# Kernel optimization log

Hardware: AMD Instinct MI355X
Metric: run time of the kernel (lower is better)

## Reference

```python
import jax, jax.numpy as jnp
import numpy as np

D_MODEL = 1024
N_HEADS = 16
D_HEAD = D_MODEL // N_HEADS
NEG_INF = -1000000000.0


def setup_inputs() -> dict:
    key = jax.random.key(0)
    ks = jax.random.split(key, 12)
    B, S1, S2 = 2, 2048, 2048
    query = jax.random.normal(ks[0], (B, S1, D_MODEL), dtype=jnp.float32)
    k_in = jax.random.normal(ks[1], (B, S2, D_MODEL), dtype=jnp.float32)
    v_in = jax.random.normal(ks[2], (B, S2, D_MODEL), dtype=jnp.float32)
    # causal mask: True = position is masked out (filled with -1e9)
    mask = jnp.broadcast_to(jnp.triu(jnp.ones((S1, S2), dtype=bool), k=1), (B, S1, S2))
    s = 1.0 / np.sqrt(D_MODEL)
    W_q = jax.random.uniform(ks[3], (D_MODEL, D_MODEL), jnp.float32, -s, s)
    b_q = jax.random.uniform(ks[4], (D_MODEL,), jnp.float32, -s, s)
    W_k = jax.random.uniform(ks[5], (D_MODEL, D_MODEL), jnp.float32, -s, s)
    b_k = jax.random.uniform(ks[6], (D_MODEL,), jnp.float32, -s, s)
    W_v = jax.random.uniform(ks[7], (D_MODEL, D_MODEL), jnp.float32, -s, s)
    b_v = jax.random.uniform(ks[8], (D_MODEL,), jnp.float32, -s, s)
    W_o = jax.random.uniform(ks[9], (D_MODEL, D_MODEL), jnp.float32, -s, s)
    b_o = jax.random.uniform(ks[10], (D_MODEL,), jnp.float32, -s, s)
    return {"query": query, "key": k_in, "value": v_in, "mask": mask,
            "W_q": W_q, "b_q": b_q, "W_k": W_k, "b_k": b_k,
            "W_v": W_v, "b_v": b_v, "W_o": W_o, "b_o": b_o}


def reference(query, key, value, mask, W_q, b_q, W_k, b_k, W_v, b_v, W_o, b_o):
    B, S1, _ = query.shape
    S2 = key.shape[1]
    scalar = 1.0 / np.sqrt(D_HEAD)
    # projections (torch Linear: x @ W.T + b)
    Q = (query @ W_q.T + b_q).reshape(B, S1, N_HEADS, D_HEAD).transpose(0, 2, 1, 3)
    K = (key @ W_k.T + b_k).reshape(B, S2, N_HEADS, D_HEAD).transpose(0, 2, 1, 3)
    V = (value @ W_v.T + b_v).reshape(B, S2, N_HEADS, D_HEAD).transpose(0, 2, 1, 3)
    # [B, H, S1, S2]
    scores = jnp.einsum('bhqd,bhkd->bhqk', Q, K) * scalar
    scores = jnp.where(mask[:, None, :, :], NEG_INF, scores)
    probs = jax.nn.softmax(scores, axis=-1)
    attn = jnp.einsum('bhqk,bhkd->bhqd', probs, V)
    concat = attn.transpose(0, 2, 1, 3).reshape(B, S1, D_MODEL)
    return concat @ W_o.T + b_o
```

## Files before the change

### kernel.cpp

```cpp
#include <hip/hip_runtime.h>
#include <hip/hip_bf16.h>
#include <stdint.h>

typedef __bf16 bf16;
typedef __bf16 bf16x8 __attribute__((ext_vector_type(8)));
typedef float f32x4 __attribute__((ext_vector_type(4)));
typedef float f32x16 __attribute__((ext_vector_type(16)));
typedef unsigned int u32;
typedef u32 u32x4 __attribute__((ext_vector_type(4)));

#define D_MODEL 1024
#define S_LEN 2048
#define NB 2
#define NH 16
#define DH 64

__device__ __forceinline__ void gload_lds16(const bf16* g, bf16* l) {
    auto gp = reinterpret_cast<const __attribute__((address_space(1))) unsigned int*>(
        reinterpret_cast<uintptr_t>(g));
    auto lp = reinterpret_cast<__attribute__((address_space(3))) unsigned int*>(
        reinterpret_cast<uintptr_t>(l));
    __builtin_amdgcn_global_load_lds(gp, lp, 16, 0, 0);
}

__device__ __forceinline__ u32 cvtpk(float lo, float hi) {
    u32 r; asm("v_cvt_pk_bf16_f32 %0, %1, %2" : "=v"(r) : "v"(lo), "v"(hi)); return r;
}
__device__ __forceinline__ void plswap(u32& a, u32& b) {
    asm("v_permlane32_swap_b32 %0, %1" : "+v"(a), "+v"(b));
}

__global__ __launch_bounds__(256)
void cvt_all(const float* __restrict__ q, const float* __restrict__ k,
             const float* __restrict__ v, const float* __restrict__ w0,
             const float* __restrict__ w1, const float* __restrict__ w2,
             const float* __restrict__ w3,
             bf16* __restrict__ oq, bf16* __restrict__ ok, bf16* __restrict__ ov,
             bf16* __restrict__ o0, bf16* __restrict__ o1, bf16* __restrict__ o2,
             bf16* __restrict__ o3)
{
    const int bid = blockIdx.x;
    const float* in; bf16* out; int local;
    if (bid < 6144) {
        int r = bid >> 11; local = bid & 2047;
        in  = (r == 0) ? q  : (r == 1) ? k  : v;
        out = (r == 0) ? oq : (r == 1) ? ok : ov;
    } else {
        int wb = bid - 6144;
        int r = wb >> 9; local = wb & 511;
        in  = (r == 0) ? w0 : (r == 1) ? w1 : (r == 2) ? w2 : w3;
        out = (r == 0) ? o0 : (r == 1) ? o1 : (r == 2) ? o2 : o3;
    }
    const size_t i = ((size_t)local * 256 + threadIdx.x) * 8;
    f32x4 x = *(const f32x4*)(in + i);
    f32x4 y = *(const f32x4*)(in + i + 4);
    bf16x8 o;
    #pragma unroll
    for (int j = 0; j < 4; ++j) { o[j] = (bf16)x[j]; o[4 + j] = (bf16)y[j]; }
    *(bf16x8*)(out + i) = o;
}

template<int OUT_F32, int TRANS>
__global__ __launch_bounds__(256)
void gemm_bf16(const bf16* __restrict__ Ap, const bf16* __restrict__ Bp,
               const float* __restrict__ bias, void* __restrict__ Cp,
               int M, int N, int K, float cscale)
{
    __shared__ __align__(16) bf16 As[2][128 * 64];
    __shared__ __align__(16) bf16 Bs[2][64 * 64];

    const int t = threadIdx.x, lane = t & 63, wid = t >> 6;
    const int nbn = N >> 6;
    const int cpx = gridDim.x >> 3;
    const int bid = blockIdx.x;
    const int swz = (bid & 7) * cpx + (bid >> 3);
    const int bm0 = (swz / nbn) << 7;
    const int bn0 = (swz % nbn) << 6;
    const int r16 = lane & 15, g = lane >> 4;
    const int wr = (wid >> 1) << 6;
    const int wc = (wid & 1) << 5;

    f32x4 acc[4][2] = {};

    auto stage = [&](int buf, int k0) {
        #pragma unroll
        for (int i = 0; i < 4; ++i) {
            int ch = wid * 256 + i * 64 + lane;
            int row = ch >> 3, c8 = ch & 7;
            int sc = c8 ^ (row & 7);
            gload_lds16(Ap + (size_t)(bm0 + row) * K + k0 + sc * 8, &As[buf][ch * 8]);
        }
        #pragma unroll
        for (int i = 0; i < 2; ++i) {
            int ch = wid * 128 + i * 64 + lane;
            int row = ch >> 3, c8 = ch & 7;
            int sc = c8 ^ (row & 7);
            gload_lds16(Bp + (size_t)(bn0 + row) * K + k0 + sc * 8, &Bs[buf][ch * 8]);
        }
    };

    int cur = 0;
    stage(0, 0);
    for (int k0 = 0; k0 < K; k0 += 64) {
        __syncthreads();
        if (k0 + 64 < K) stage(cur ^ 1, k0 + 64);
        #pragma unroll
        for (int ks = 0; ks < 2; ++ks) {
            const int cl = ks * 4 + g;
            bf16x8 af[4], bfr[2];
            #pragma unroll
            for (int mi = 0; mi < 4; ++mi) {
                int row = wr + mi * 16 + r16;
                af[mi] = *(const bf16x8*)((const char*)&As[cur][0] + row * 128 + ((cl ^ (row & 7)) << 4));
            }
            #pragma unroll
            for (int ni = 0; ni < 2; ++ni) {
                int row = wc + ni * 16 + r16;
                bfr[ni] = *(const bf16x8*)((const char*)&Bs[cur][0] + row * 128 + ((cl ^ (row & 7)) << 4));
            }
            #pragma unroll
            for (int mi = 0; mi < 4; ++mi)
                #pragma unroll
                for (int ni = 0; ni < 2; ++ni)
                    acc[mi][ni] = __builtin_amdgcn_mfma_f32_16x16x32_bf16(af[mi], bfr[ni], acc[mi][ni], 0, 0, 0);
        }
        cur ^= 1;
    }

    const int rb = g * 4;
    if (TRANS) {
        __syncthreads();
        bf16* Ts = (bf16*)&As[0][0];
        #pragma unroll
        for (int mi = 0; mi < 4; ++mi)
            #pragma unroll
            for (int ni = 0; ni < 2; ++ni) {
                int dl = wc + ni * 16 + r16;
                float bv = bias[bn0 + dl];
                #pragma unroll
                for (int r = 0; r < 4; ++r) {
                    int sl = wr + mi * 16 + rb + r;
                    Ts[dl * 136 + sl] = (bf16)(acc[mi][ni][r] + bv);
                }
            }
        __syncthreads();
        const int bq = bm0 >> 11, hq = bn0 >> 6, s0 = bm0 & 2047;
        bf16* VT = (bf16*)Cp;
        #pragma unroll
        for (int i2 = 0; i2 < 4; ++i2) {
            int ch = t + i2 * 256;
            int d = ch >> 4, sc = ch & 15;
            bf16x8 v = *(const bf16x8*)&Ts[d * 136 + sc * 8];
            *(bf16x8*)(VT + ((size_t)(bq * 16 + hq) * 64 + d) * S_LEN + s0 + sc * 8) = v;
        }
    } else {
        #pragma unroll
        for (int mi = 0; mi < 4; ++mi) {
            #pragma unroll
            for (int ni = 0; ni < 2; ++ni) {
                int cg = bn0 + wc + ni * 16 + r16;
                float bv = bias[cg];
                #pragma unroll
                for (int r = 0; r < 4; ++r) {
                    int rg = bm0 + wr + mi * 16 + rb + r;
                    float v = (acc[mi][ni][r] + bv) * cscale;
                    if (OUT_F32) ((float*)Cp)[(size_t)rg * N + cg] = v;
                    else         ((bf16*)Cp)[(size_t)rg * N + cg] = (bf16)v;
                }
            }
        }
    }
}

__global__ __launch_bounds__(256, 2)
void attn5(const bf16* __restrict__ Qp, const bf16* __restrict__ Kp,
           const bf16* __restrict__ VTp, bf16* __restrict__ Op)
{
    __shared__ __align__(16) char smem[32768];

    const int t = threadIdx.x, lane = t & 63, qs = t >> 6;
    const int l31 = lane & 31, hh = lane >> 5;

    const int bid = blockIdx.x;
    const int xcd = bid & 7, slot = bid >> 3;
    const int bh = xcd * 4 + (slot & 3);
    const int sh = slot >> 2;
    const int qt = (sh < 8) ? (15 - sh) : (sh - 8);
    const int b = bh >> 4, h = bh & 15;

    const size_t base = (size_t)b * (S_LEN * D_MODEL) + h * DH;
    const size_t vtbase = (size_t)bh * (DH * S_LEN);

    const int q0b = qt * 128;
    const int q0w = q0b + qs * 32;
    const int NT = 2 * qt + 2;
    const int teff = 2 * qt + (qs >> 1) + 1;

    const int ch0 = t, ch1 = t + 256;
    const int row0 = ch0 >> 3, ssc0 = ((ch0 & 7) ^ (row0 & 7)) << 3;
    const int row1 = ch1 >> 3, ssc1 = ((ch1 & 7) ^ (row1 & 7)) << 3;

    auto stage = [&](int buf, int tt) {
        char* kb = smem + buf * 16384;
        char* vb = kb + 8192;
        gload_lds16(Kp + base + (size_t)(tt * 64 + row0) * D_MODEL + ssc0, (bf16*)(kb + ch0 * 16));
        gload_lds16(Kp + base + (size_t)(tt * 64 + row1) * D_MODEL + ssc1, (bf16*)(kb + ch1 * 16));
        gload_lds16(VTp + vtbase + (size_t)row0 * S_LEN + tt * 64 + ssc0, (bf16*)(vb + ch0 * 16));
        gload_lds16(VTp + vtbase + (size_t)row1 * S_LEN + tt * 64 + ssc1, (bf16*)(vb + ch1 * 16));
    };

    bf16x8 qf[4];
    {
        const bf16* qrow = Qp + base + (size_t)(q0w + l31) * D_MODEL + hh * 8;
        #pragma unroll
        for (int db = 0; db < 4; ++db) qf[db] = *(const bf16x8*)(qrow + db * 16);
    }

    f32x16 oacc[2] = {};
    float mx = -1e30f, lsum = 0.f;

    int cur = 0;
    stage(0, 0);
    #pragma unroll 1
    for (int tt = 0; tt < NT; ++tt) {
        __syncthreads();
        if (tt + 1 < NT) stage(cur ^ 1, tt + 1);
        if (tt < teff) {
            const char* kbp = smem + cur * 16384;
            const char* vbp = kbp + 8192;
            f32x16 sacc[2] = {};
            __builtin_amdgcn_s_setprio(1);
            #pragma unroll
            for (int ks = 0; ks < 2; ++ks)
                #pragma unroll
                for (int db = 0; db < 4; ++db) {
                    int row = ks * 32 + l31, c = db * 2 + hh;
                    bf16x8 kf = *(const bf16x8*)(kbp + row * 128 + ((c ^ (row & 7)) << 4));
                    sacc[ks] = __builtin_amdgcn_mfma_f32_32x32x16_bf16(kf, qf[db], sacc[ks], 0, 0, 0);
                }
            __builtin_amdgcn_s_setprio(0);
            bf16x8 vf[8];
            #pragma unroll
            for (int kb2 = 0; kb2 < 4; ++kb2)
                #pragma unroll
                for (int dt = 0; dt < 2; ++dt) {
                    int row = dt * 32 + l31, c = kb2 * 2 + hh;
                    vf[kb2 * 2 + dt] = *(const bf16x8*)(vbp + row * 128 + ((c ^ (row & 7)) << 4));
                }
            if (tt == teff - 1) {
                const int thr = q0w + l31 - 4 * hh - tt * 64;
                #pragma unroll
                for (int ks = 0; ks < 2; ++ks)
                    #pragma unroll
                    for (int r2 = 0; r2 < 16; ++r2) {
                        const int cr = 32 * ks + (r2 & 3) + 8 * (r2 >> 2);
                        if (cr > thr) sacc[ks][r2] = -1e9f;
                    }
            }
            float pm = -3e38f;
            #pragma unroll
            for (int ks = 0; ks < 2; ++ks)
                #pragma unroll
                for (int r2 = 0; r2 < 16; ++r2) pm = fmaxf(pm, sacc[ks][r2]);
            pm = fmaxf(pm, __shfl_xor(pm, 32));
            float mnew = fmaxf(mx, pm);
            float al = __builtin_exp2f(mx - mnew);
            float ts = 0.f;
            #pragma unroll
            for (int ks = 0; ks < 2; ++ks)
                #pragma unroll
                for (int r2 = 0; r2 < 16; ++r2) {
                    float p = __builtin_exp2f(sacc[ks][r2] - mnew);
                    sacc[ks][r2] = p;
                    ts += p;
                }
            ts += __shfl_xor(ts, 32);
            lsum = lsum * al + ts;
            mx = mnew;
            #pragma unroll
            for (int dt = 0; dt < 2; ++dt)
                #pragma unroll
                for (int r2 = 0; r2 < 16; ++r2) oacc[dt][r2] *= al;

            #pragma unroll
            for (int kb2 = 0; kb2 < 4; ++kb2) {
                const int ks = kb2 >> 1, rb2 = (kb2 & 1) * 8;
                u32 w0 = cvtpk(sacc[ks][rb2 + 0], sacc[ks][rb2 + 1]);
                u32 w2 = cvtpk(sacc[ks][rb2 + 4], sacc[ks][rb2 + 5]);
                u32 w1 = cvtpk(sacc[ks][rb2 + 2], sacc[ks][rb2 + 3]);
                u32 w3 = cvtpk(sacc[ks][rb2 + 6], sacc[ks][rb2 + 7]);
                plswap(w0, w2);
                plswap(w1, w3);
                u32x4 pw; pw[0] = w0; pw[1] = w1; pw[2] = w2; pw[3] = w3;
                bf16x8 pb = __builtin_bit_cast(bf16x8, pw);
                __builtin_amdgcn_s_setprio(1);
                #pragma unroll
                for (int dt = 0; dt < 2; ++dt)
                    oacc[dt] = __builtin_amdgcn_mfma_f32_32x32x16_bf16(vf[kb2 * 2 + dt], pb, oacc[dt], 0, 0, 0);
                __builtin_amdgcn_s_setprio(0);
            }
        }
        cur ^= 1;
    }

    __syncthreads();
    {
        const float inv = 1.0f / lsum;
        char* Os = smem;
        #pragma unroll
        for (int dt = 0; dt < 2; ++dt)
            #pragma unroll
            for (int r2 = 0; r2 < 16; r2 += 2) {
                int d = dt * 32 + (r2 & 3) + 8 * (r2 >> 2) + 4 * hh;
                u32 w = cvtpk(oacc[dt][r2] * inv, oacc[dt][r2 + 1] * inv);
                *(u32*)(Os + (qs * 32 + l31) * 136 + d * 2) = w;
            }
    }
    __syncthreads();
    #pragma unroll
    for (int i2 = 0; i2 < 4; ++i2) {
        int ch2 = t + i2 * 256;
        int qrow = ch2 >> 3, c8 = ch2 & 7;
        bf16x8 v = *(const bf16x8*)(smem + qrow * 136 + c8 * 16);
        *(bf16x8*)(Op + base + (size_t)(q0b + qrow) * D_MODEL + c8 * 8) = v;
    }
}

extern "C" void kernel_launch(void* const* d_in, const int* in_sizes, int n_in,
                              void* d_out, int out_size, void* d_ws, size_t ws_size,
                              hipStream_t stream)
{
    const float* query = (const float*)d_in[0];
    const float* key   = (const float*)d_in[1];
    const float* value = (const float*)d_in[2];
    const float* W_q = (const float*)d_in[4];
    const float* b_q = (const float*)d_in[5];
    const float* W_k = (const float*)d_in[6];
    const float* b_k = (const float*)d_in[7];
    const float* W_v = (const float*)d_in[8];
    const float* b_v = (const float*)d_in[9];
    const float* W_o = (const float*)d_in[10];
    const float* b_o = (const float*)d_in[11];

    const int M = NB * S_LEN;
    char* w = (char*)d_ws;
    const size_t MB = 1 << 20;
    bf16* qbf = (bf16*)(w);
    bf16* kbf = (bf16*)(w + 8 * MB);
    bf16* vbf = (bf16*)(w + 16 * MB);
    bf16* Qb  = (bf16*)(w + 24 * MB);
    bf16* Kb  = (bf16*)(w + 32 * MB);
    bf16* VT  = (bf16*)(w + 40 * MB);
    bf16* Wqb = (bf16*)(w + 48 * MB);
    bf16* Wkb = (bf16*)(w + 50 * MB);
    bf16* Wvb = (bf16*)(w + 52 * MB);
    bf16* Wob = (bf16*)(w + 54 * MB);
    bf16* Ob  = qbf;

    dim3 blk(256);
    cvt_all<<<dim3(8192), blk, 0, stream>>>(query, key, value, W_q, W_k, W_v, W_o,
                                            qbf, kbf, vbf, Wqb, Wkb, Wvb, Wob);

    dim3 gproj((M / 128) * (D_MODEL / 64));
    const float qscale = 0.125f * 1.4426950408889634f;
    gemm_bf16<0, 0><<<gproj, blk, 0, stream>>>(qbf, Wqb, b_q, Qb, M, D_MODEL, D_MODEL, qscale);
    gemm_bf16<0, 0><<<gproj, blk, 0, stream>>>(kbf, Wkb, b_k, Kb, M, D_MODEL, D_MODEL, 1.0f);
    gemm_bf16<0, 1><<<gproj, blk, 0, stream>>>(vbf, Wvb, b_v, VT, M, D_MODEL, D_MODEL, 1.0f);

    attn5<<<dim3(512), blk, 0, stream>>>(Qb, Kb, VT, Ob);

    gemm_bf16<1, 0><<<gproj, blk, 0, stream>>>(Ob, Wob, b_o, d_out, M, D_MODEL, D_MODEL, 1.0f);
}
```

Before: 115.2 us.

## Fuse QKV projections into one launch and split attention over KV halves

Merges the three projection GEMMs into a single 1536-block launch that selects Q, K or V per column tile. The attention kernel now splits each query tile's KV range into two halves across 1024 blocks (split-K flash decoding), writing unnormalized partial outputs plus max and sum to workspace, and a new merge kernel combines them. It also skips the rescale when no lane's row max grows, loads V fragments lazily to cut register pressure, and raises occupancy to 3 blocks per CU. The aim is better load balance and fewer launches, at the cost of an extra kernel and extra workspace traffic.

```diff
diff --git a/kernel.cpp b/kernel.cpp
--- a/kernel.cpp
+++ b/kernel.cpp
@@ -60,17 +60,134 @@
     *(bf16x8*)(out + i) = o;
 }
 
-template<int OUT_F32, int TRANS>
 __global__ __launch_bounds__(256)
-void gemm_bf16(const bf16* __restrict__ Ap, const bf16* __restrict__ Bp,
-               const float* __restrict__ bias, void* __restrict__ Cp,
-               int M, int N, int K, float cscale)
+void gemm_qkv(const bf16* __restrict__ Aq, const bf16* __restrict__ Ak, const bf16* __restrict__ Av,
+              const bf16* __restrict__ Wq, const bf16* __restrict__ Wk, const bf16* __restrict__ Wv,
+              const float* __restrict__ bq, const float* __restrict__ bk, const float* __restrict__ bv,
+              bf16* __restrict__ Qo, bf16* __restrict__ Ko, bf16* __restrict__ VTo, float qscale)
 {
     __shared__ __align__(16) bf16 As[2][128 * 64];
     __shared__ __align__(16) bf16 Bs[2][64 * 64];
 
+    const int K = 1024;
     const int t = threadIdx.x, lane = t & 63, wid = t >> 6;
-    const int nbn = N >> 6;
+    const int nbn = 48;
+    const int cpx = gridDim.x >> 3;
+    const int bid = blockIdx.x;
+    const int swz = (bid & 7) * cpx + (bid >> 3);
+    const int bm0 = (swz / nbn) << 7;
+    const int bn0 = (swz % nbn) << 6;
+    const int sel = bn0 >> 10;
+    const int nl  = bn0 & 1023;
+    const bf16* Ap = (sel == 0) ? Aq : (sel == 1) ? Ak : Av;
+    const bf16* Bp = (sel == 0) ? Wq : (sel == 1) ? Wk : Wv;
+    const float* bias = (sel == 0) ? bq : (sel == 1) ? bk : bv;
+
+    const int r16 = lane & 15, g = lane >> 4;
+    const int wr = (wid >> 1) << 6;
+    const int wc = (wid & 1) << 5;
+
+    f32x4 acc[4][2] = {};
+
+    auto stage = [&](int buf, int k0) {
+        #pragma unroll
+        for (int i = 0; i < 4; ++i) {
+            int ch = wid * 256 + i * 64 + lane;
+            int row = ch >> 3, c8 = ch & 7;
+            int sc = c8 ^ (row & 7);
+            gload_lds16(Ap + (size_t)(bm0 + row) * K + k0 + sc * 8, &As[buf][ch * 8]);
+        }
+        #pragma unroll
+        for (int i = 0; i < 2; ++i) {
+            int ch = wid * 128 + i * 64 + lane;
+            int row = ch >> 3, c8 = ch & 7;
+            int sc = c8 ^ (row & 7);
+            gload_lds16(Bp + (size_t)(nl + row) * K + k0 + sc * 8, &Bs[buf][ch * 8]);
+        }
+    };
+
+    int cur = 0;
+    stage(0, 0);
+    for (int k0 = 0; k0 < K; k0 += 64) {
+        __syncthreads();
+        if (k0 + 64 < K) stage(cur ^ 1, k0 + 64);
+        #pragma unroll
+        for (int ks = 0; ks < 2; ++ks) {
+            const int cl = ks * 4 + g;
+            bf16x8 af[4], bfr[2];
+            #pragma unroll
+            for (int mi = 0; mi < 4; ++mi) {
+                int row = wr + mi * 16 + r16;
+                af[mi] = *(const bf16x8*)((const char*)&As[cur][0] + row * 128 + ((cl ^ (row & 7)) << 4));
+            }
+            #pragma unroll
+            for (int ni = 0; ni < 2; ++ni) {
+                int row = wc + ni * 16 + r16;
+                bfr[ni] = *(const bf16x8*)((const char*)&Bs[cur][0] + row * 128 + ((cl ^ (row & 7)) << 4));
+            }
+            #pragma unroll
+            for (int mi = 0; mi < 4; ++mi)
+                #pragma unroll
+                for (int ni = 0; ni < 2; ++ni)
+                    acc[mi][ni] = __builtin_amdgcn_mfma_f32_16x16x32_bf16(af[mi], bfr[ni], acc[mi][ni], 0, 0, 0);
+        }
+        cur ^= 1;
+    }
+
+    const int rb = g * 4;
+    if (sel == 2) {
+        __syncthreads();
+        bf16* Ts = (bf16*)&As[0][0];
+        #pragma unroll
+        for (int mi = 0; mi < 4; ++mi)
+            #pragma unroll
+            for (int ni = 0; ni < 2; ++ni) {
+                int dl = wc + ni * 16 + r16;
+                float bv = bias[nl + dl];
+                #pragma unroll
+                for (int r = 0; r < 4; ++r) {
+                    int sl = wr + mi * 16 + rb + r;
+                    Ts[dl * 136 + sl] = (bf16)(acc[mi][ni][r] + bv);
+                }
+            }
+        __syncthreads();
+        const int bq2 = bm0 >> 11, hq = nl >> 6, s0 = bm0 & 2047;
+        #pragma unroll
+        for (int i2 = 0; i2 < 4; ++i2) {
+            int ch = t + i2 * 256;
+            int d = ch >> 4, sc = ch & 15;
+            bf16x8 v = *(const bf16x8*)&Ts[d * 136 + sc * 8];
+            *(bf16x8*)(VTo + ((size_t)(bq2 * 16 + hq) * 64 + d) * S_LEN + s0 + sc * 8) = v;
+        }
+    } else {
+        bf16* out = sel ? Ko : Qo;
+        const float cs = sel ? 1.0f : qscale;
+        #pragma unroll
+        for (int mi = 0; mi < 4; ++mi) {
+            #pragma unroll
+            for (int ni = 0; ni < 2; ++ni) {
+                int cg = nl + wc + ni * 16 + r16;
+                float bv = bias[cg];
+                #pragma unroll
+                for (int r = 0; r < 4; ++r) {
+                    int rg = bm0 + wr + mi * 16 + rb + r;
+                    out[(size_t)rg * 1024 + cg] = (bf16)((acc[mi][ni][r] + bv) * cs);
+                }
+            }
+        }
+    }
+}
+
+__global__ __launch_bounds__(256)
+void gemm_out(const bf16* __restrict__ Ap, const bf16* __restrict__ Bp,
+              const float* __restrict__ bias, float* __restrict__ Cp)
+{
+    __shared__ __align__(16) bf16 As[2][128 * 64];
+    __shared__ __align__(16) bf16 Bs[2][64 * 64];
+
+    const int K = 1024, N = 1024;
+    const int t = threadIdx.x, lane = t & 63, wid = t >> 6;
+    const int nbn = 16;
     const int cpx = gridDim.x >> 3;
     const int bid = blockIdx.x;
     const int swz = (bid & 7) * cpx + (bid >> 3);
@@ -128,64 +245,36 @@
     }
 
     const int rb = g * 4;
-    if (TRANS) {
-        __syncthreads();
-        bf16* Ts = (bf16*)&As[0][0];
-        #pragma unroll
-        for (int mi = 0; mi < 4; ++mi)
-            #pragma unroll
-            for (int ni = 0; ni < 2; ++ni) {
-                int dl = wc + ni * 16 + r16;
-                float bv = bias[bn0 + dl];
-                #pragma unroll
-                for (int r = 0; r < 4; ++r) {
-                    int sl = wr + mi * 16 + rb + r;
-                    Ts[dl * 136 + sl] = (bf16)(acc[mi][ni][r] + bv);
-                }
-            }
-        __syncthreads();
-        const int bq = bm0 >> 11, hq = bn0 >> 6, s0 = bm0 & 2047;
-        bf16* VT = (bf16*)Cp;
-        #pragma unroll
-        for (int i2 = 0; i2 < 4; ++i2) {
-            int ch = t + i2 * 256;
-            int d = ch >> 4, sc = ch & 15;
-            bf16x8 v = *(const bf16x8*)&Ts[d * 136 + sc * 8];
-            *(bf16x8*)(VT + ((size_t)(bq * 16 + hq) * 64 + d) * S_LEN + s0 + sc * 8) = v;
-        }
-    } else {
-        #pragma unroll
-        for (int mi = 0; mi < 4; ++mi) {
-            #pragma unroll
-            for (int ni = 0; ni < 2; ++ni) {
-                int cg = bn0 + wc + ni * 16 + r16;
-                float bv = bias[cg];
-                #pragma unroll
-                for (int r = 0; r < 4; ++r) {
-                    int rg = bm0 + wr + mi * 16 + rb + r;
-                    float v = (acc[mi][ni][r] + bv) * cscale;
-                    if (OUT_F32) ((float*)Cp)[(size_t)rg * N + cg] = v;
-                    else         ((bf16*)Cp)[(size_t)rg * N + cg] = (bf16)v;
-                }
-            }
-        }
-    }
-}
-
-__global__ __launch_bounds__(256, 2)
-void attn5(const bf16* __restrict__ Qp, const bf16* __restrict__ Kp,
-           const bf16* __restrict__ VTp, bf16* __restrict__ Op)
-{
-    __shared__ __align__(16) char smem[32768];
+    #pragma unroll
+    for (int mi = 0; mi < 4; ++mi) {
+        #pragma unroll
+        for (int ni = 0; ni < 2; ++ni) {
+            int cg = bn0 + wc + ni * 16 + r16;
+            float bv = bias[cg];
+            #pragma unroll
+            for (int r = 0; r < 4; ++r) {
+                int rg = bm0 + wr + mi * 16 + rb + r;
+                Cp[(size_t)rg * N + cg] = acc[mi][ni][r] + bv;
+            }
+        }
+    }
+}
+
+__global__ __launch_bounds__(256, 3)
+void attn7(const bf16* __restrict__ Qp, const bf16* __restrict__ Kp,
+           const bf16* __restrict__ VTp, bf16* __restrict__ Pws, float* __restrict__ MLws)
+{
+    __shared__ __align__(16) char smem[2][16384];
 
     const int t = threadIdx.x, lane = t & 63, qs = t >> 6;
     const int l31 = lane & 31, hh = lane >> 5;
 
     const int bid = blockIdx.x;
-    const int xcd = bid & 7, slot = bid >> 3;
-    const int bh = xcd * 4 + (slot & 3);
-    const int sh = slot >> 2;
-    const int qt = (sh < 8) ? (15 - sh) : (sh - 8);
+    const int xcd = bid & 7, s = bid >> 3;
+    const int bh = xcd * 4 + (s >> 5);
+    const int kh = (s >> 4) & 1;
+    const int im = s & 15, g2 = im >> 2, r4 = im & 3;
+    const int qt = (r4 == 0) ? 15 - g2 : (r4 == 1) ? 7 - g2 : (r4 == 2) ? g2 : 8 + g2;
     const int b = bh >> 4, h = bh & 15;
 
     const size_t base = (size_t)b * (S_LEN * D_MODEL) + h * DH;
@@ -193,20 +282,21 @@
 
     const int q0b = qt * 128;
     const int q0w = q0b + qs * 32;
-    const int NT = 2 * qt + 2;
+    const int rounds = qt + 1;
+    const int tbase = kh ? (qt + 1) : 0;
     const int teff = 2 * qt + (qs >> 1) + 1;
 
-    const int ch0 = t, ch1 = t + 256;
-    const int row0 = ch0 >> 3, ssc0 = ((ch0 & 7) ^ (row0 & 7)) << 3;
-    const int row1 = ch1 >> 3, ssc1 = ((ch1 & 7) ^ (row1 & 7)) << 3;
-
     auto stage = [&](int buf, int tt) {
-        char* kb = smem + buf * 16384;
+        char* kb = smem[buf];
         char* vb = kb + 8192;
-        gload_lds16(Kp + base + (size_t)(tt * 64 + row0) * D_MODEL + ssc0, (bf16*)(kb + ch0 * 16));
-        gload_lds16(Kp + base + (size_t)(tt * 64 + row1) * D_MODEL + ssc1, (bf16*)(kb + ch1 * 16));
-        gload_lds16(VTp + vtbase + (size_t)row0 * S_LEN + tt * 64 + ssc0, (bf16*)(vb + ch0 * 16));
-        gload_lds16(VTp + vtbase + (size_t)row1 * S_LEN + tt * 64 + ssc1, (bf16*)(vb + ch1 * 16));
+        #pragma unroll
+        for (int p = 0; p < 2; ++p) {
+            int ch = t + p * 256;
+            int row = ch >> 3, c8 = ch & 7;
+            int so = (c8 ^ (row & 7)) << 3;
+            gload_lds16(Kp + base + (size_t)(tt * 64 + row) * D_MODEL + so, (bf16*)(kb + ch * 16));
+            gload_lds16(VTp + vtbase + (size_t)row * S_LEN + tt * 64 + so, (bf16*)(vb + ch * 16));
+        }
     };
 
     bf16x8 qf[4];
@@ -220,33 +310,28 @@
     float mx = -1e30f, lsum = 0.f;
 
     int cur = 0;
-    stage(0, 0);
+    stage(0, tbase);
     #pragma unroll 1
-    for (int tt = 0; tt < NT; ++tt) {
+    for (int r = 0; r < rounds; ++r) {
         __syncthreads();
-        if (tt + 1 < NT) stage(cur ^ 1, tt + 1);
+        if (r + 1 < rounds) stage(cur ^ 1, tbase + r + 1);
+        const int tt = tbase + r;
         if (tt < teff) {
-            const char* kbp = smem + cur * 16384;
+            const char* kbp = smem[cur];
             const char* vbp = kbp + 8192;
             f32x16 sacc[2] = {};
             __builtin_amdgcn_s_setprio(1);
             #pragma unroll
-            for (int ks = 0; ks < 2; ++ks)
+            for (int ks = 0; ks < 2; ++ks) {
+                int row = ks * 32 + l31;
                 #pragma unroll
                 for (int db = 0; db < 4; ++db) {
-                    int row = ks * 32 + l31, c = db * 2 + hh;
+                    int c = db * 2 + hh;
                     bf16x8 kf = *(const bf16x8*)(kbp + row * 128 + ((c ^ (row & 7)) << 4));
                     sacc[ks] = __builtin_amdgcn_mfma_f32_32x32x16_bf16(kf, qf[db], sacc[ks], 0, 0, 0);
                 }
+            }
             __builtin_amdgcn_s_setprio(0);
-            bf16x8 vf[8];
-            #pragma unroll
-            for (int kb2 = 0; kb2 < 4; ++kb2)
-                #pragma unroll
-                for (int dt = 0; dt < 2; ++dt) {
-                    int row = dt * 32 + l31, c = kb2 * 2 + hh;
-                    vf[kb2 * 2 + dt] = *(const bf16x8*)(vbp + row * 128 + ((c ^ (row & 7)) << 4));
-                }
             if (tt == teff - 1) {
                 const int thr = q0w + l31 - 4 * hh - tt * 64;
                 #pragma unroll
@@ -263,24 +348,26 @@
                 #pragma unroll
                 for (int r2 = 0; r2 < 16; ++r2) pm = fmaxf(pm, sacc[ks][r2]);
             pm = fmaxf(pm, __shfl_xor(pm, 32));
-            float mnew = fmaxf(mx, pm);
-            float al = __builtin_exp2f(mx - mnew);
+            if (__any(pm > mx)) {
+                float mnew = fmaxf(mx, pm);
+                float al = __builtin_exp2f(mx - mnew);
+                lsum *= al;
+                #pragma unroll
+                for (int dt = 0; dt < 2; ++dt)
+                    #pragma unroll
+                    for (int r2 = 0; r2 < 16; ++r2) oacc[dt][r2] *= al;
+                mx = mnew;
+            }
             float ts = 0.f;
             #pragma unroll
             for (int ks = 0; ks < 2; ++ks)
                 #pragma unroll
                 for (int r2 = 0; r2 < 16; ++r2) {
-                    float p = __builtin_exp2f(sacc[ks][r2] - mnew);
+                    float p = __builtin_exp2f(sacc[ks][r2] - mx);
                     sacc[ks][r2] = p;
                     ts += p;
                 }
-            ts += __shfl_xor(ts, 32);
-            lsum = lsum * al + ts;
-            mx = mnew;
-            #pragma unroll
-            for (int dt = 0; dt < 2; ++dt)
-                #pragma unroll
-                for (int r2 = 0; r2 < 16; ++r2) oacc[dt][r2] *= al;
+            lsum += ts + __shfl_xor(ts, 32);
 
             #pragma unroll
             for (int kb2 = 0; kb2 < 4; ++kb2) {
@@ -295,34 +382,69 @@
                 bf16x8 pb = __builtin_bit_cast(bf16x8, pw);
                 __builtin_amdgcn_s_setprio(1);
                 #pragma unroll
-                for (int dt = 0; dt < 2; ++dt)
-                    oacc[dt] = __builtin_amdgcn_mfma_f32_32x32x16_bf16(vf[kb2 * 2 + dt], pb, oacc[dt], 0, 0, 0);
+                for (int dt = 0; dt < 2; ++dt) {
+                    int row = dt * 32 + l31, c = kb2 * 2 + hh;
+                    bf16x8 vfr = *(const bf16x8*)(vbp + row * 128 + ((c ^ (row & 7)) << 4));
+                    oacc[dt] = __builtin_amdgcn_mfma_f32_32x32x16_bf16(vfr, pb, oacc[dt], 0, 0, 0);
+                }
                 __builtin_amdgcn_s_setprio(0);
             }
         }
         cur ^= 1;
     }
 
-    __syncthreads();
-    {
-        const float inv = 1.0f / lsum;
-        char* Os = smem;
-        #pragma unroll
-        for (int dt = 0; dt < 2; ++dt)
-            #pragma unroll
-            for (int r2 = 0; r2 < 16; r2 += 2) {
-                int d = dt * 32 + (r2 & 3) + 8 * (r2 >> 2) + 4 * hh;
-                u32 w = cvtpk(oacc[dt][r2] * inv, oacc[dt][r2 + 1] * inv);
-                *(u32*)(Os + (qs * 32 + l31) * 136 + d * 2) = w;
-            }
-    }
-    __syncthreads();
+    bf16* pb = Pws + (size_t)bid * 8192;
+    const int qrow = qs * 32 + l31;
     #pragma unroll
-    for (int i2 = 0; i2 < 4; ++i2) {
-        int ch2 = t + i2 * 256;
-        int qrow = ch2 >> 3, c8 = ch2 & 7;
-        bf16x8 v = *(const bf16x8*)(smem + qrow * 136 + c8 * 16);
-        *(bf16x8*)(Op + base + (size_t)(q0b + qrow) * D_MODEL + c8 * 8) = v;
+    for (int dt = 0; dt < 2; ++dt)
+        #pragma unroll
+        for (int r2 = 0; r2 < 16; r2 += 2) {
+            int d = dt * 32 + (r2 & 3) + 8 * (r2 >> 2) + 4 * hh;
+            *(u32*)(pb + qrow * 64 + d) = cvtpk(oacc[dt][r2], oacc[dt][r2 + 1]);
+        }
+    if (hh == 0) {
+        MLws[(size_t)bid * 256 + qrow] = mx;
+        MLws[(size_t)bid * 256 + 128 + qrow] = lsum;
+    }
+}
+
+__global__ __launch_bounds__(256)
+void attn_merge(const bf16* __restrict__ Pws, const float* __restrict__ MLws,
+                bf16* __restrict__ Ob)
+{
+    const int mb = blockIdx.x;
+    const int bh = mb >> 4, qt = mb & 15;
+    const int xcd = bh >> 2;
+    int i;
+    if (qt >= 12)      i = (15 - qt) * 4;
+    else if (qt >= 8)  i = (qt - 8) * 4 + 3;
+    else if (qt >= 4)  i = (7 - qt) * 4 + 1;
+    else               i = qt * 4 + 2;
+    const int sA = (bh & 3) * 32 + i;
+    const int bidA = sA * 8 + xcd;
+    const int bidB = (sA + 16) * 8 + xcd;
+    const int b = bh >> 4, h = bh & 15;
+
+    const int t = threadIdx.x;
+    const int q = t >> 1, dh = t & 1;
+    const float mA = MLws[(size_t)bidA * 256 + q], lA = MLws[(size_t)bidA * 256 + 128 + q];
+    const float mB = MLws[(size_t)bidB * 256 + q], lB = MLws[(size_t)bidB * 256 + 128 + q];
+    const float m = fmaxf(mA, mB);
+    float a0 = __builtin_exp2f(mA - m), a1 = __builtin_exp2f(mB - m);
+    const float linv = 1.0f / (lA * a0 + lB * a1);
+    a0 *= linv; a1 *= linv;
+    const bf16* pA = Pws + (size_t)bidA * 8192 + q * 64 + dh * 32;
+    const bf16* pB = Pws + (size_t)bidB * 8192 + q * 64 + dh * 32;
+    bf16* op = Ob + (size_t)(b * S_LEN + qt * 128 + q) * D_MODEL + h * DH + dh * 32;
+    #pragma unroll
+    for (int j = 0; j < 4; ++j) {
+        bf16x8 va = *(const bf16x8*)(pA + j * 8);
+        bf16x8 vb = *(const bf16x8*)(pB + j * 8);
+        bf16x8 o;
+        #pragma unroll
+        for (int e = 0; e < 8; ++e)
+            o[e] = (bf16)(a0 * (float)va[e] + a1 * (float)vb[e]);
+        *(bf16x8*)(op + j * 8) = o;
     }
 }
 
@@ -342,7 +464,6 @@
     const float* W_o = (const float*)d_in[10];
     const float* b_o = (const float*)d_in[11];
 
-    const int M = NB * S_LEN;
     char* w = (char*)d_ws;
     const size_t MB = 1 << 20;
     bf16* qbf = (bf16*)(w);
@@ -355,19 +476,20 @@
     bf16* Wkb = (bf16*)(w + 50 * MB);
     bf16* Wvb = (bf16*)(w + 52 * MB);
     bf16* Wob = (bf16*)(w + 54 * MB);
-    bf16* Ob  = qbf;
+    bf16*  Pws  = (bf16*)(w);
+    float* MLws = (float*)(w + 16 * MB);
+    bf16*  Ob   = (bf16*)(w + 17 * MB);
 
     dim3 blk(256);
     cvt_all<<<dim3(8192), blk, 0, stream>>>(query, key, value, W_q, W_k, W_v, W_o,
                                             qbf, kbf, vbf, Wqb, Wkb, Wvb, Wob);
 
-    dim3 gproj((M / 128) * (D_MODEL / 64));
     const float qscale = 0.125f * 1.4426950408889634f;
-    gemm_bf16<0, 0><<<gproj, blk, 0, stream>>>(qbf, Wqb, b_q, Qb, M, D_MODEL, D_MODEL, qscale);
-    gemm_bf16<0, 0><<<gproj, blk, 0, stream>>>(kbf, Wkb, b_k, Kb, M, D_MODEL, D_MODEL, 1.0f);
-    gemm_bf16<0, 1><<<gproj, blk, 0, stream>>>(vbf, Wvb, b_v, VT, M, D_MODEL, D_MODEL, 1.0f);
-
-    attn5<<<dim3(512), blk, 0, stream>>>(Qb, Kb, VT, Ob);
-
-    gemm_bf16<1, 0><<<gproj, blk, 0, stream>>>(Ob, Wob, b_o, d_out, M, D_MODEL, D_MODEL, 1.0f);
-}
+    gemm_qkv<<<dim3(1536), blk, 0, stream>>>(qbf, kbf, vbf, Wqb, Wkb, Wvb,
+                                             b_q, b_k, b_v, Qb, Kb, VT, qscale);
+
+    attn7<<<dim3(1024), blk, 0, stream>>>(Qb, Kb, VT, Pws, MLws);
+    attn_merge<<<dim3(512), blk, 0, stream>>>(Pws, MLws, Ob);
+
+    gemm_out<<<dim3(512), blk, 0, stream>>>(Ob, Wob, b_o, (float*)d_out);
+}
```

New measurement: 130.1 us. +13.0%, slower.
